# Kernel optimization log

Measured on AMD Instinct MI355X. Metric: run time of the kernel, lower is better.

The kernel has to match this reference:

```python
import jax, jax.numpy as jnp
import numpy as np

IN_C = 128
MID_C = 128
EPS = 1e-5


def layer_norm(x, g, b):
    mu = jnp.mean(x, axis=-1, keepdims=True)
    var = jnp.mean(jnp.square(x - mu), axis=-1, keepdims=True)
    return (x - mu) * jax.lax.rsqrt(var + EPS) * g + b


def setup_inputs() -> dict:
    key = jax.random.key(0)
    ks = jax.random.split(key, 16)
    B, N = 1, 384
    s_in = 1.0 / np.sqrt(IN_C)
    s_mid = 1.0 / np.sqrt(MID_C)
    return {
        "x2d": jax.random.normal(ks[0], (B, N, N, IN_C), dtype=jnp.float32),
        "n1_g": jnp.ones((IN_C,), jnp.float32),
        "n1_b": jnp.zeros((IN_C,), jnp.float32),
        "n2_g": jnp.ones((MID_C,), jnp.float32),
        "n2_b": jnp.zeros((MID_C,), jnp.float32),
        "w1i": jax.random.uniform(ks[1], (MID_C, IN_C), jnp.float32, -s_in, s_in),
        "b1i": jnp.zeros((MID_C,), jnp.float32),
        "w1j": jax.random.uniform(ks[2], (MID_C, IN_C), jnp.float32, -s_in, s_in),
        "b1j": jnp.zeros((MID_C,), jnp.float32),
        "w1i_s": jax.random.uniform(ks[3], (MID_C, IN_C), jnp.float32, -s_in, s_in),
        "b1i_s": jnp.zeros((MID_C,), jnp.float32),
        "w1j_s": jax.random.uniform(ks[4], (MID_C, IN_C), jnp.float32, -s_in, s_in),
        "b1j_s": jnp.zeros((MID_C,), jnp.float32),
        "w2": jax.random.uniform(ks[5], (IN_C, MID_C), jnp.float32, -s_mid, s_mid),
        "b2": jnp.zeros((IN_C,), jnp.float32),
        "w3": jax.random.uniform(ks[6], (IN_C, IN_C), jnp.float32, -s_in, s_in),
        "b3": jnp.zeros((IN_C,), jnp.float32),
    }


def reference(x2d, n1_g, n1_b, n2_g, n2_b, w1i, b1i, w1j, b1j,
              w1i_s, b1i_s, w1j_s, b1j_s, w2, b2, w3, b3):
    # x2d: [B, N, N, C]
    x = layer_norm(x2d, n1_g, n1_b)
    i = (x @ w1i.T + b1i) * jax.nn.sigmoid(x @ w1i_s.T + b1i_s)  # [B,N,N,mid]
    j = (x @ w1j.T + b1j) * jax.nn.sigmoid(x @ w1j_s.T + b1j_s)  # [B,N,N,mid]
    out = jnp.einsum('bikc,bjkc->bijc', i, j)                    # contract over k
    out = layer_norm(out, n2_g, n2_b)
    out = out @ w2.T + b2
    out = out * jax.nn.sigmoid(x @ w3.T + b3)
    return out
```

## Files before the change

### kernel.cpp

```cpp
#include <hip/hip_runtime.h>

#define NN 384
#define CC 128
#define NPOS (NN * NN)
#define TPB 4

typedef short bf8_t __attribute__((ext_vector_type(8)));
typedef float f32x4_t __attribute__((ext_vector_type(4)));

#define MFMA16(a, b, c) __builtin_amdgcn_mfma_f32_16x16x32_bf16((a), (b), (c), 0, 0, 0)

__device__ __forceinline__ unsigned short f2bf(float f) {
  unsigned int u = __builtin_bit_cast(unsigned int, f);
  u += 0x7fffu + ((u >> 16) & 1u);
  return (unsigned short)(u >> 16);
}
__device__ __forceinline__ float bf2f(unsigned short s) {
  return __builtin_bit_cast(float, ((unsigned int)s) << 16);
}
__device__ __forceinline__ float sigm(float x) {
  float e = __builtin_amdgcn_exp2f(x * -1.44269504f);
  return __builtin_amdgcn_rcpf(1.0f + e);
}

__global__ __launch_bounds__(256) void kW(const float* __restrict__ a,
                                          const float* __restrict__ b,
                                          const float* __restrict__ c,
                                          const float* __restrict__ d,
                                          const float* __restrict__ e,
                                          const float* __restrict__ f,
                                          unsigned short* __restrict__ o) {
  int idx = (blockIdx.x * 256 + threadIdx.x) * 4;
  const float* s = f;
  if (idx < 16384) s = a;
  else if (idx < 32768) s = b;
  else if (idx < 49152) s = c;
  else if (idx < 65536) s = d;
  else if (idx < 81920) s = e;
  int off = idx & 16383;
  float4 v = *(const float4*)(s + off);
  o[idx + 0] = f2bf(v.x);
  o[idx + 1] = f2bf(v.y);
  o[idx + 2] = f2bf(v.z);
  o[idx + 3] = f2bf(v.w);
}

__global__ __launch_bounds__(256) void kLN(const float* __restrict__ x,
                                           const float* __restrict__ n1g,
                                           const float* __restrict__ n1b,
                                           unsigned short* __restrict__ x_ln) {
  int t = threadIdx.x;
  int pos = blockIdx.x * 128 + (t >> 1);
  int half = t & 1;
  const float* xr = x + (size_t)pos * CC + half * 64;
  float v[64];
  float s = 0.f;
#pragma unroll
  for (int a = 0; a < 16; ++a) {
    float4 f4 = ((const float4*)xr)[a];
    v[4 * a + 0] = f4.x; v[4 * a + 1] = f4.y;
    v[4 * a + 2] = f4.z; v[4 * a + 3] = f4.w;
    s += f4.x + f4.y + f4.z + f4.w;
  }
  s += __shfl_xor(s, 1);
  float mu = s * (1.0f / CC);
  float vs = 0.f;
#pragma unroll
  for (int a = 0; a < 64; ++a) { float d = v[a] - mu; vs += d * d; }
  vs += __shfl_xor(vs, 1);
  float rs = rsqrtf(vs * (1.0f / CC) + 1e-5f);
  unsigned short* dst = x_ln + (size_t)pos * CC + half * 64;
#pragma unroll
  for (int a8 = 0; a8 < 8; ++a8) {
    union { bf8_t v8; unsigned short e[8]; } u;
#pragma unroll
    for (int e = 0; e < 8; ++e) {
      int c = half * 64 + a8 * 8 + e;
      u.e[e] = f2bf((v[a8 * 8 + e] - mu) * rs * n1g[c] + n1b[c]);
    }
    *(bf8_t*)(dst + a8 * 8) = u.v8;
  }
}

__global__ __launch_bounds__(256, 2) void kP(
    const unsigned short* __restrict__ x_ln, const unsigned short* __restrict__ wcat,
    const float* __restrict__ b1i, const float* __restrict__ b1is,
    const float* __restrict__ b1j, const float* __restrict__ b1js,
    const float* __restrict__ b3v, unsigned short* __restrict__ i_s,
    unsigned short* __restrict__ j_s, unsigned short* __restrict__ g3) {
  __shared__ __align__(16) unsigned short lds[24832];
  unsigned short* gt = lds + 16384;
  float* bl = (float*)(lds + 24576);

  int b = blockIdx.x;
  int xcd = b & 7, m = b >> 3;
  int group = m / 6, job = m % 6;
  int p = job >> 1, h = job & 1;
  int t = threadIdx.x, lane = t & 63, wave = t >> 6;
  int lr = lane & 15, lh = lane >> 4;

  const unsigned short* Wv = wcat + (size_t)(p < 2 ? p * 2 : 4) * CC * CC + h * 64 * CC;
#pragma unroll
  for (int it = 0; it < 4; ++it) {
    int u = it * 256 + t;
    int row = u >> 4, sl = u & 15;
    int slg = sl ^ (row & 7);
    __builtin_amdgcn_global_load_lds(
        (const __attribute__((address_space(1))) unsigned int*)(Wv + row * CC + slg * 8),
        (__attribute__((address_space(3))) unsigned int*)(lds + u * 8), 16, 0, 0);
  }
  if (p < 2) {
    const unsigned short* Wg = Wv + CC * CC;
#pragma unroll
    for (int it = 0; it < 4; ++it) {
      int u = it * 256 + t;
      int row = u >> 4, sl = u & 15;
      int slg = sl ^ (row & 7);
      __builtin_amdgcn_global_load_lds(
          (const __attribute__((address_space(1))) unsigned int*)(Wg + row * CC + slg * 8),
          (__attribute__((address_space(3))) unsigned int*)(lds + 8192 + u * 8), 16, 0, 0);
    }
  }
  if (p < 2) {
    const float* bvp = p ? b1j : b1i;
    const float* bgp = p ? b1js : b1is;
    if (t < 16) ((float4*)bl)[t] = ((const float4*)(bvp + h * 64))[t];
    else if (t < 32) ((float4*)bl)[t] = ((const float4*)(bgp + h * 64))[t - 16];
  } else {
    if (t < 16) ((float4*)bl)[t] = ((const float4*)(b3v + h * 64))[t];
  }

  int pt0 = xcd * 144 + group * TPB;
  bf8_t xfA[2][4], xfB[2][4];
#define LOADXF(xf, tt)                                                               \
  {                                                                                  \
    int p0l = (pt0 + (tt)) * 128;                                                    \
    _Pragma("unroll") for (int nt = 0; nt < 2; ++nt)                                 \
        _Pragma("unroll") for (int kk = 0; kk < 4; ++kk)                             \
            xf[nt][kk] = *(const bf8_t*)(x_ln +                                      \
                                         (size_t)(p0l + wave * 32 + nt * 16 + lr) *  \
                                             CC + kk * 32 + lh * 8);                 \
  }
  LOADXF(xfA, 0);
  __syncthreads();

  f32x4_t z4 = {0.f, 0.f, 0.f, 0.f};
#pragma unroll
  for (int tt = 0; tt < TPB; ++tt) {
    int p0 = (pt0 + tt) * 128;
    bf8_t(&xfc)[2][4] = (tt & 1) ? xfB : xfA;
    bf8_t(&xfn)[2][4] = (tt & 1) ? xfA : xfB;
    if (tt + 1 < TPB) LOADXF(xfn, tt + 1);

    f32x4_t accV[2][4], accG[2][4];
#pragma unroll
    for (int nt = 0; nt < 2; ++nt)
#pragma unroll
      for (int ct = 0; ct < 4; ++ct) { accV[nt][ct] = z4; accG[nt][ct] = z4; }
    if (p < 2) {
#pragma unroll
      for (int ct = 0; ct < 4; ++ct)
#pragma unroll
        for (int kk = 0; kk < 4; ++kk) {
          int rv = ct * 16 + lr;
          int slot = (kk * 4 + lh) ^ (rv & 7);
          bf8_t wv = *(const bf8_t*)&lds[rv * 128 + slot * 8];
          bf8_t wg = *(const bf8_t*)&lds[8192 + rv * 128 + slot * 8];
#pragma unroll
          for (int nt = 0; nt < 2; ++nt) {
            accV[nt][ct] = MFMA16(wv, xfc[nt][kk], accV[nt][ct]);
            accG[nt][ct] = MFMA16(wg, xfc[nt][kk], accG[nt][ct]);
          }
        }
    } else {
#pragma unroll
      for (int ct = 0; ct < 4; ++ct)
#pragma unroll
        for (int kk = 0; kk < 4; ++kk) {
          int rv = ct * 16 + lr;
          int slot = (kk * 4 + lh) ^ (rv & 7);
          bf8_t wv = *(const bf8_t*)&lds[rv * 128 + slot * 8];
#pragma unroll
          for (int nt = 0; nt < 2; ++nt)
            accV[nt][ct] = MFMA16(xfc[nt][kk], wv, accV[nt][ct]);
        }
    }

    if (p < 2) {
#pragma unroll
      for (int nt = 0; nt < 2; ++nt)
#pragma unroll
        for (int ct = 0; ct < 4; ++ct)
#pragma unroll
          for (int r = 0; r < 4; ++r) {
            int cl = ct * 16 + lh * 4 + r;
            int pos = wave * 32 + nt * 16 + lr;
            float o = (accV[nt][ct][r] + bl[cl]) * sigm(accG[nt][ct][r] + bl[64 + cl]);
            int sw = ((ct * 4 + lh) & 7) << 4;
            gt[cl * 128 + (pos ^ sw)] = f2bf(o);
          }
      __syncthreads();
      unsigned short* dstm = p ? j_s : i_s;
#pragma unroll
      for (int it = 0; it < 4; ++it) {
        int u = it * 256 + t;
        int cl = u >> 4, ch = u & 15;
        int s = (cl >> 2) & 7;
        bf8_t v = *(const bf8_t*)&gt[cl * 128 + ((ch ^ (s << 1)) * 8)];
        *(bf8_t*)(dstm + (size_t)(h * 64 + cl) * NPOS + p0 + ch * 8) = v;
      }
    } else {
#pragma unroll
      for (int nt = 0; nt < 2; ++nt)
#pragma unroll
        for (int ct = 0; ct < 4; ++ct)
#pragma unroll
          for (int r = 0; r < 4; ++r) {
            int pos = wave * 32 + nt * 16 + lh * 4 + r;
            int cl = ct * 16 + lr;
            float o = sigm(accV[nt][ct][r] + bl[cl]);
            int slot = (cl >> 3) ^ (pos & 7);
            gt[pos * 64 + slot * 8 + (cl & 7)] = f2bf(o);
          }
      __syncthreads();
#pragma unroll
      for (int it = 0; it < 4; ++it) {
        int u = it * 256 + t;
        int pos = u >> 3, ch = u & 7;
        int slot = ch ^ (pos & 7);
        bf8_t v = *(const bf8_t*)&gt[pos * 64 + slot * 8];
        *(bf8_t*)(g3 + (size_t)(p0 + pos) * CC + h * 64 + ch * 8) = v;
      }
    }
    __syncthreads();
  }
}

__global__ __launch_bounds__(256) void kB(const unsigned short* __restrict__ i_s,
                                          const unsigned short* __restrict__ j_s,
                                          unsigned short* __restrict__ out_pre) {
  __shared__ unsigned short At[128][32];
  __shared__ unsigned short Bt[128][32];
  int b = blockIdx.x;
  int logical = (b & 7) * 144 + (b >> 3);
  int c = logical / 9;
  int tt = logical % 9;
  int i0 = (tt / 3) * 128, j0 = (tt % 3) * 128;
  const unsigned short* Ab = i_s + ((size_t)c * NN + i0) * NN;
  const unsigned short* Bb = j_s + ((size_t)c * NN + j0) * NN;
  int t = threadIdx.x, lane = t & 63, wave = t >> 6;
  int wi = (wave >> 1) * 64, wj = (wave & 1) * 64;
  int lr = lane & 15, lh = lane >> 4;
  int rsub = lane >> 2;
  int ksub = (lane & 3) * 8;

  f32x4_t z4 = {0.f, 0.f, 0.f, 0.f};
  f32x4_t acc[4][4];
#pragma unroll
  for (int mt = 0; mt < 4; ++mt)
#pragma unroll
    for (int nt = 0; nt < 4; ++nt) acc[mt][nt] = z4;

  for (int k0 = 0; k0 < NN; k0 += 32) {
#pragma unroll
    for (int half = 0; half < 2; ++half) {
      int r = half * 64 + wave * 16;
      __builtin_amdgcn_global_load_lds(
          (const __attribute__((address_space(1))) unsigned int*)(Ab + (size_t)(r + rsub) * NN + k0 + ksub),
          (__attribute__((address_space(3))) unsigned int*)&At[r][0], 16, 0, 0);
      __builtin_amdgcn_global_load_lds(
          (const __attribute__((address_space(1))) unsigned int*)(Bb + (size_t)(r + rsub) * NN + k0 + ksub),
          (__attribute__((address_space(3))) unsigned int*)&Bt[r][0], 16, 0, 0);
    }
    __syncthreads();
    bf8_t af2[4], bf2[4];
#pragma unroll
    for (int mt = 0; mt < 4; ++mt) af2[mt] = *(const bf8_t*)&At[wi + mt * 16 + lr][lh * 8];
#pragma unroll
    for (int nt = 0; nt < 4; ++nt) bf2[nt] = *(const bf8_t*)&Bt[wj + nt * 16 + lr][lh * 8];
#pragma unroll
    for (int mt = 0; mt < 4; ++mt)
#pragma unroll
      for (int nt = 0; nt < 4; ++nt) acc[mt][nt] = MFMA16(af2[mt], bf2[nt], acc[mt][nt]);
    __syncthreads();
  }
  unsigned short* orow = out_pre + ((size_t)c * NN + (i0 + wi)) * NN + (j0 + wj);
#pragma unroll
  for (int mt = 0; mt < 4; ++mt)
#pragma unroll
    for (int nt = 0; nt < 4; ++nt)
#pragma unroll
      for (int r = 0; r < 4; ++r)
        orow[(size_t)(mt * 16 + lh * 4 + r) * NN + nt * 16 + lr] = f2bf(acc[mt][nt][r]);
}

__global__ __launch_bounds__(256, 2) void kC(const unsigned short* __restrict__ out_pre,
                                             const float* __restrict__ n2g,
                                             const float* __restrict__ n2b,
                                             const unsigned short* __restrict__ w2bf,
                                             const float* __restrict__ b2,
                                             const unsigned short* __restrict__ g3,
                                             float* __restrict__ out) {
  __shared__ __align__(16) unsigned short ldsu[17408];
  int b = blockIdx.x;
  int ii = b / 3, j0 = (b % 3) * 128;
  int t = threadIdx.x, lane = t & 63, wave = t >> 6;

#pragma unroll
  for (int it = 0; it < 8; ++it) {
    int u = it * 256 + t;
    int c = u >> 4, jg = u & 15;
    __builtin_amdgcn_global_load_lds(
        (const __attribute__((address_space(1))) unsigned int*)(out_pre + ((size_t)c * NN + ii) * NN + j0 + jg * 8),
        (__attribute__((address_space(3))) unsigned int*)(ldsu + u * 8), 16, 0, 0);
  }
  __syncthreads();

  {
    int pos = t >> 1, half = t & 1;
    float v[64];
    float s = 0.f;
#pragma unroll
    for (int a = 0; a < 64; ++a) { v[a] = bf2f(ldsu[(half * 64 + a) * 128 + pos]); s += v[a]; }
    s += __shfl_xor(s, 1);
    float mu = s * (1.0f / CC);
    float vs = 0.f;
#pragma unroll
    for (int a = 0; a < 64; ++a) { float d = v[a] - mu; vs += d * d; }
    vs += __shfl_xor(vs, 1);
    float rs = rsqrtf(vs * (1.0f / CC) + 1e-5f);
    union { bf8_t v8[8]; unsigned short e[64]; } u;
#pragma unroll
    for (int a = 0; a < 64; ++a) {
      int c = half * 64 + a;
      u.e[a] = f2bf((v[a] - mu) * rs * n2g[c] + n2b[c]);
    }
    __syncthreads();
#pragma unroll
    for (int a8 = 0; a8 < 8; ++a8)
      *(bf8_t*)&ldsu[pos * 136 + half * 64 + a8 * 8] = u.v8[a8];
  }
  __syncthreads();

  int lr = lane & 15, lh = lane >> 4;
  bf8_t af2[2][4];
#pragma unroll
  for (int mt = 0; mt < 2; ++mt)
#pragma unroll
    for (int kk = 0; kk < 4; ++kk)
      af2[mt][kk] = *(const bf8_t*)&ldsu[(wave * 32 + mt * 16 + lr) * 136 + kk * 32 + lh * 8];
  f32x4_t z4 = {0.f, 0.f, 0.f, 0.f};
  f32x4_t acc[2][8];
#pragma unroll
  for (int mt = 0; mt < 2; ++mt)
#pragma unroll
    for (int nt = 0; nt < 8; ++nt) acc[mt][nt] = z4;
#pragma unroll
  for (int nt = 0; nt < 8; ++nt) {
#pragma unroll
    for (int kk = 0; kk < 4; ++kk) {
      bf8_t bw = *(const bf8_t*)(w2bf + (size_t)(nt * 16 + lr) * CC + kk * 32 + lh * 8);
#pragma unroll
      for (int mt = 0; mt < 2; ++mt) acc[mt][nt] = MFMA16(af2[mt][kk], bw, acc[mt][nt]);
    }
  }
#pragma unroll
  for (int mt = 0; mt < 2; ++mt)
#pragma unroll
    for (int nt = 0; nt < 8; ++nt)
#pragma unroll
      for (int r = 0; r < 4; ++r) {
        int posl = wave * 32 + mt * 16 + lh * 4 + r;
        int c = nt * 16 + lr;
        size_t p = (size_t)ii * NN + j0 + posl;
        float y = acc[mt][nt][r] + b2[c];
        out[p * CC + c] = y * bf2f(g3[p * CC + c]);
      }
}

extern "C" void kernel_launch(void* const* d_in, const int* in_sizes, int n_in,
                              void* d_out, int out_size, void* d_ws, size_t ws_size,
                              hipStream_t stream) {
  (void)in_sizes; (void)n_in; (void)out_size; (void)ws_size;
  const float* x2d  = (const float*)d_in[0];
  const float* n1g  = (const float*)d_in[1];
  const float* n1b  = (const float*)d_in[2];
  const float* n2g  = (const float*)d_in[3];
  const float* n2b  = (const float*)d_in[4];
  const float* w1i  = (const float*)d_in[5];
  const float* b1i  = (const float*)d_in[6];
  const float* w1j  = (const float*)d_in[7];
  const float* b1j  = (const float*)d_in[8];
  const float* w1is = (const float*)d_in[9];
  const float* b1is = (const float*)d_in[10];
  const float* w1js = (const float*)d_in[11];
  const float* b1js = (const float*)d_in[12];
  const float* w2   = (const float*)d_in[13];
  const float* b2   = (const float*)d_in[14];
  const float* w3   = (const float*)d_in[15];
  const float* b3   = (const float*)d_in[16];

  char* ws = (char*)d_ws;
  unsigned short* wcat = (unsigned short*)ws;
  size_t TELEMS = (size_t)CC * NN * NN;
  unsigned short* i_s  = (unsigned short*)(ws + 262144);
  unsigned short* j_s  = i_s + TELEMS;
  unsigned short* g3   = j_s + TELEMS;
  unsigned short* x_ln = g3 + TELEMS;
  unsigned short* out_pre = x_ln;
  float* outp = (float*)d_out;

  kW<<<96, 256, 0, stream>>>(w1i, w1is, w1j, w1js, w3, w2, wcat);
  kLN<<<1152, 256, 0, stream>>>(x2d, n1g, n1b, x_ln);
  kP<<<1728, 256, 0, stream>>>(x_ln, wcat, b1i, b1is, b1j, b1js, b3, i_s, j_s, g3);
  kB<<<1152, 256, 0, stream>>>(i_s, j_s, out_pre);
  kC<<<1152, 256, 0, stream>>>(out_pre, n2g, n2b, wcat + 5 * CC * CC, b2, g3, outp);
}
```

Before: 176.6 us.

## Double-buffer kB LDS tiles and stage output through swizzled LDS for coalesced stores

The batched GEMM kernel kB now double-buffers its A/B k-slices in LDS. The next slice's global_load_lds is issued before the MFMAs on the current slice, so there is one barrier per iteration instead of two. The epilogue writes bf16 results into an XOR-swizzled LDS tile and then stores 16-byte coalesced rows to global memory, replacing scattered 2-byte stores. This doubles the LDS footprint to 32 KB and adds an extra barrier plus an LDS round trip at the end.

After: 174.4 us. Within noise of the previous version (-1.3%).

```diff
diff --git a/kernel.cpp b/kernel.cpp
--- a/kernel.cpp
+++ b/kernel.cpp
@@ -239,8 +239,7 @@
 __global__ __launch_bounds__(256) void kB(const unsigned short* __restrict__ i_s,
                                           const unsigned short* __restrict__ j_s,
                                           unsigned short* __restrict__ out_pre) {
-  __shared__ unsigned short At[128][32];
-  __shared__ unsigned short Bt[128][32];
+  __shared__ __align__(16) unsigned short lds[16384];
   int b = blockIdx.x;
   int logical = (b & 7) * 144 + (b >> 3);
   int c = logical / 9;
@@ -254,44 +253,64 @@
   int rsub = lane >> 2;
   int ksub = (lane & 3) * 8;
 
-  f32x4_t z4 = {0.f, 0.f, 0.f, 0.f};
-  f32x4_t acc[4][4];
-#pragma unroll
-  for (int mt = 0; mt < 4; ++mt)
-#pragma unroll
-    for (int nt = 0; nt < 4; ++nt) acc[mt][nt] = z4;
-
-  for (int k0 = 0; k0 < NN; k0 += 32) {
+  auto ISSUE = [&](int ks, int bsel) {
+    int k0 = ks * 32;
 #pragma unroll
     for (int half = 0; half < 2; ++half) {
       int r = half * 64 + wave * 16;
       __builtin_amdgcn_global_load_lds(
           (const __attribute__((address_space(1))) unsigned int*)(Ab + (size_t)(r + rsub) * NN + k0 + ksub),
-          (__attribute__((address_space(3))) unsigned int*)&At[r][0], 16, 0, 0);
+          (__attribute__((address_space(3))) unsigned int*)(lds + bsel * 4096 + r * 32), 16, 0, 0);
       __builtin_amdgcn_global_load_lds(
           (const __attribute__((address_space(1))) unsigned int*)(Bb + (size_t)(r + rsub) * NN + k0 + ksub),
-          (__attribute__((address_space(3))) unsigned int*)&Bt[r][0], 16, 0, 0);
-    }
-    __syncthreads();
+          (__attribute__((address_space(3))) unsigned int*)(lds + 8192 + bsel * 4096 + r * 32), 16, 0, 0);
+    }
+  };
+
+  f32x4_t z4 = {0.f, 0.f, 0.f, 0.f};
+  f32x4_t acc[4][4];
+#pragma unroll
+  for (int mt = 0; mt < 4; ++mt)
+#pragma unroll
+    for (int nt = 0; nt < 4; ++nt) acc[mt][nt] = z4;
+
+  ISSUE(0, 0);
+  __syncthreads();
+  for (int ks = 0; ks < 12; ++ks) {
+    if (ks < 11) ISSUE(ks + 1, (ks + 1) & 1);
+    const unsigned short* At = lds + (ks & 1) * 4096;
+    const unsigned short* Bt = lds + 8192 + (ks & 1) * 4096;
     bf8_t af2[4], bf2[4];
 #pragma unroll
-    for (int mt = 0; mt < 4; ++mt) af2[mt] = *(const bf8_t*)&At[wi + mt * 16 + lr][lh * 8];
-#pragma unroll
-    for (int nt = 0; nt < 4; ++nt) bf2[nt] = *(const bf8_t*)&Bt[wj + nt * 16 + lr][lh * 8];
+    for (int mt = 0; mt < 4; ++mt) af2[mt] = *(const bf8_t*)&At[(wi + mt * 16 + lr) * 32 + lh * 8];
+#pragma unroll
+    for (int nt = 0; nt < 4; ++nt) bf2[nt] = *(const bf8_t*)&Bt[(wj + nt * 16 + lr) * 32 + lh * 8];
 #pragma unroll
     for (int mt = 0; mt < 4; ++mt)
 #pragma unroll
       for (int nt = 0; nt < 4; ++nt) acc[mt][nt] = MFMA16(af2[mt], bf2[nt], acc[mt][nt]);
     __syncthreads();
   }
-  unsigned short* orow = out_pre + ((size_t)c * NN + (i0 + wi)) * NN + (j0 + wj);
+
 #pragma unroll
   for (int mt = 0; mt < 4; ++mt)
 #pragma unroll
     for (int nt = 0; nt < 4; ++nt)
 #pragma unroll
-      for (int r = 0; r < 4; ++r)
-        orow[(size_t)(mt * 16 + lh * 4 + r) * NN + nt * 16 + lr] = f2bf(acc[mt][nt][r]);
+      for (int r = 0; r < 4; ++r) {
+        int i = wi + mt * 16 + lh * 4 + r;
+        int j = wj + nt * 16 + lr;
+        lds[i * 128 + (((j >> 3) ^ (i & 7)) * 8) + (j & 7)] = f2bf(acc[mt][nt][r]);
+      }
+  __syncthreads();
+  unsigned short* obase = out_pre + ((size_t)c * NN + i0) * NN + j0;
+#pragma unroll
+  for (int it = 0; it < 8; ++it) {
+    int g = it * 256 + t;
+    int row = g >> 4, gsl = g & 15;
+    bf8_t v = *(const bf8_t*)&lds[row * 128 + ((gsl ^ (row & 7)) * 8)];
+    *(bf8_t*)(obase + (size_t)row * NN + gsl * 8) = v;
+  }
 }
 
 __global__ __launch_bounds__(256, 2) void kC(const unsigned short* __restrict__ out_pre,
```
